# Kernel optimization log

Hardware: AMD Instinct MI355X
Metric: run time of the kernel (lower is better)

The kernel has to match this reference:

```python
import jax, jax.numpy as jnp
import numpy as np

N = 524288   # total spokes
D = 128      # dim_hidden
B = 128      # graphs in batch
H = 64       # hubs per graph (static, num_hubs_type='S')
K = 4        # hubs_per_spoke


def setup_inputs() -> dict:
    key = jax.random.key(0)
    ks = jax.random.split(key, 5)
    x = jax.random.normal(ks[0], (N, D), jnp.float32)
    spoke_init_hub_idx = jax.random.randint(ks[1], (N,), 0, H)
    batch_idx = jnp.sort(jax.random.randint(ks[2], (N,), 0, B))
    s1 = 1.0 / np.sqrt(D)
    s2 = 1.0 / np.sqrt(2 * D)
    W1 = jax.random.uniform(ks[3], (D, 2 * D), jnp.float32, -s1, s1)
    b1 = jnp.zeros((2 * D,), jnp.float32)
    W2 = jax.random.uniform(ks[4], (2 * D, D), jnp.float32, -s2, s2)
    b2 = jnp.zeros((D,), jnp.float32)
    return {"x": x, "spoke_init_hub_idx": spoke_init_hub_idx, "batch_idx": batch_idx,
            "W1": W1, "b1": b1, "W2": W2, "b2": b2}


def reference(x, spoke_init_hub_idx, batch_idx, W1, b1, W2, b2):
    # FeedForward on spokes: Linear -> GELU(exact, torch default) -> Linear
    h = jax.nn.gelu(x @ W1 + b1, approximate=False) @ W2 + b2  # [N, D]

    # batched hub index: local hub idx offset by graph (uniform H hubs/graph)
    gidx = batch_idx * H + spoke_init_hub_idx  # [N]

    # scatter_mean of spoke features into hubs (empty hubs -> 0, as torch scatter_mean)
    sums = jax.ops.segment_sum(h, gidx, num_segments=B * H)                    # [B*H, D]
    cnt = jax.ops.segment_sum(jnp.ones((N,), h.dtype), gidx, num_segments=B * H)
    hub_features = sums / jnp.maximum(cnt, 1.0)[:, None]                       # [B*H, D]

    # assign each spoke to the K hubs closest to its initial hub (within its graph)
    hf = hub_features.reshape(B, H, D)
    d2 = jnp.sum((hf[:, :, None, :] - hf[:, None, :, :]) ** 2, axis=-1)        # [B, H, H]
    _, knn = jax.lax.top_k(-d2, K)                                             # [B, H, K] local hub ids
    hubs_idx = knn[batch_idx, spoke_init_hub_idx] + batch_idx[:, None] * H     # [N, K] global hub ids
    spokes_idx = jnp.repeat(jnp.arange(N), K)
    spokes_hubs_edge_index = jnp.stack([spokes_idx, hubs_idx.reshape(-1)], axis=0)  # [2, N*K]

    return hub_features, spokes_hubs_edge_index
```

## Files before the change

### kernel.cpp

```cpp
#include <hip/hip_runtime.h>
#include <hip/hip_bf16.h>

#define N_SPOKES 524288
#define DIM      128
#define DIM2     256
#define NB       128
#define NH       64
#define BH       8192

#define OUT_HF   0
#define OUT_E0   1048576
#define OUT_E1   3145728

typedef __attribute__((ext_vector_type(8))) short  short8;
typedef __attribute__((ext_vector_type(4))) float  float4v;
typedef __attribute__((ext_vector_type(4))) unsigned short ushort4v;

__device__ inline unsigned short f2bf(float f) {
    __hip_bfloat16 h = __float2bfloat16(f);
    return *reinterpret_cast<unsigned short*>(&h);
}

__device__ inline float gelu_f(float v) {
    float s = v * (1.0f + 0.044715f * v * v);
    float e = __builtin_exp2f(-2.302118131f * s);
    return v * __builtin_amdgcn_rcpf(1.0f + e);
}

__global__ void setup_kernel(const int* __restrict__ batchidx, const int* __restrict__ hubidx,
                             const float* __restrict__ W1,
                             unsigned short* __restrict__ w1t,
                             int* __restrict__ goff, int* __restrict__ cnt) {
    int b = blockIdx.x, tid = threadIdx.x;
    if (b < 2048) {
        int i = b * 256 + tid;
        if (i < N_SPOKES) {
            int bi = batchidx[i];
            int bp = (i == 0) ? -1 : batchidx[i - 1];
            for (int g = bp + 1; g <= bi; ++g) goff[g] = i;
            if (i == N_SPOKES - 1)
                for (int g = bi + 1; g <= NB; ++g) goff[g] = N_SPOKES;
            atomicAdd(&cnt[bi * NH + hubidx[i]], 1);
        }
    } else {
        int idx = (b - 2048) * 256 + tid;
        if (idx < DIM * DIM2) {
            int n = idx >> 7, k = idx & 127;
            w1t[idx] = f2bf(W1[k * DIM2 + n]);
        }
    }
}

__launch_bounds__(512, 2)
__global__ void ffn_fused(const float* __restrict__ x,
                          const int* __restrict__ hubidx,
                          const int* __restrict__ goff,
                          const unsigned short* __restrict__ w1t,
                          const float* __restrict__ b1,
                          float* __restrict__ outbuf,
                          int atomic_mode) {
    __shared__ unsigned short sA[128 * 136];
    __shared__ unsigned short sU[256 * 136];
    __shared__ int sHub[128];

    const int tid  = threadIdx.x;
    const int lane = tid & 63;
    const int w    = tid >> 6;
    const int c_lo = lane & 15;
    const int c_hi = lane >> 4;
    const int wcb  = w * 32;
    const int g      = blockIdx.x >> 1;
    const int cchunk = blockIdx.x & 1;

    const int s = goff[g], e = goff[g + 1];
    const int len = e - s;
    const int cs  = (len + 1) >> 1;
    const int ms  = s + cchunk * cs;
    int me = ms + cs; if (me > e) me = e;
    const int n  = me - ms;
    const int nt = (n + 127) >> 7;

    short8 bfr[2][4];
    #pragma unroll
    for (int n4 = 0; n4 < 2; ++n4)
        #pragma unroll
        for (int k = 0; k < 4; ++k) {
            int col = wcb + n4 * 16 + c_lo;
            bfr[n4][k] = *(const short8*)(w1t + col * DIM + k * 32 + c_hi * 8);
        }
    float bcol[2];
    #pragma unroll
    for (int n4 = 0; n4 < 2; ++n4) bcol[n4] = b1[wcb + n4 * 16 + c_lo];

    float4v hacc[4][2];
    #pragma unroll
    for (int mt = 0; mt < 4; ++mt)
        #pragma unroll
        for (int n4 = 0; n4 < 2; ++n4) hacc[mt][n4] = (float4v){0.f, 0.f, 0.f, 0.f};

    const float4v* x4 = (const float4v*)x;

    float4v pf[8];
    if (nt > 0) {
        #pragma unroll
        for (int it = 0; it < 8; ++it) {
            int f = it * 512 + tid;
            int r = f >> 5;
            int rr = r < n ? r : n - 1;
            pf[it] = x4[(size_t)(ms + rr) * 32 + (f & 31)];
        }
    }

    for (int t = 0; t < nt; ++t) {
        #pragma unroll
        for (int it = 0; it < 8; ++it) {
            int f = it * 512 + tid;
            int row = f >> 5, c4 = f & 31;
            float4v v = pf[it];
            ushort4v u = { f2bf(v.x), f2bf(v.y), f2bf(v.z), f2bf(v.w) };
            *(ushort4v*)&sA[row * 136 + c4 * 4] = u;
        }
        if (tid < 128) {
            int r = t * 128 + tid;
            sHub[tid] = (r < n) ? hubidx[ms + r] : -1;
        }
        __syncthreads();

        if (t + 1 < nt) {
            #pragma unroll
            for (int it = 0; it < 8; ++it) {
                int f = it * 512 + tid;
                int r = (t + 1) * 128 + (f >> 5);
                int rr = r < n ? r : n - 1;
                pf[it] = x4[(size_t)(ms + rr) * 32 + (f & 31)];
            }
        }

        float4v acc[8][2];
        #pragma unroll
        for (int m = 0; m < 8; ++m)
            #pragma unroll
            for (int n4 = 0; n4 < 2; ++n4) acc[m][n4] = (float4v){0.f, 0.f, 0.f, 0.f};

        #pragma unroll
        for (int k = 0; k < 4; ++k)
            #pragma unroll
            for (int m = 0; m < 8; ++m) {
                short8 a = *(const short8*)&sA[(m * 16 + c_lo) * 136 + k * 32 + c_hi * 8];
                #pragma unroll
                for (int n4 = 0; n4 < 2; ++n4)
                    acc[m][n4] = __builtin_amdgcn_mfma_f32_16x16x32_bf16(a, bfr[n4][k], acc[m][n4], 0, 0, 0);
            }

        #pragma unroll
        for (int m = 0; m < 8; ++m) {
            int rbase = m * 16 + c_hi * 4;
            #pragma unroll
            for (int n4 = 0; n4 < 2; ++n4) {
                int col = wcb + n4 * 16 + c_lo;
                float4v a4 = acc[m][n4];
                ushort4v u;
                u.x = f2bf(gelu_f(a4.x + bcol[n4]));
                u.y = f2bf(gelu_f(a4.y + bcol[n4]));
                u.z = f2bf(gelu_f(a4.z + bcol[n4]));
                u.w = f2bf(gelu_f(a4.w + bcol[n4]));
                *(ushort4v*)&sU[col * 136 + rbase] = u;
            }
        }

        #pragma unroll
        for (int ks = 0; ks < 4; ++ks) {
            int4 h0v = *(const int4*)&sHub[ks * 32 + c_hi * 8];
            int4 h1v = *(const int4*)&sHub[ks * 32 + c_hi * 8 + 4];
            short8 aS[4];
            #pragma unroll
            for (int mt = 0; mt < 4; ++mt) {
                int hb = mt * 16 + c_lo;
                short8 a;
                a[0] = (h0v.x == hb) ? (short)0x3F80 : (short)0;
                a[1] = (h0v.y == hb) ? (short)0x3F80 : (short)0;
                a[2] = (h0v.z == hb) ? (short)0x3F80 : (short)0;
                a[3] = (h0v.w == hb) ? (short)0x3F80 : (short)0;
                a[4] = (h1v.x == hb) ? (short)0x3F80 : (short)0;
                a[5] = (h1v.y == hb) ? (short)0x3F80 : (short)0;
                a[6] = (h1v.z == hb) ? (short)0x3F80 : (short)0;
                a[7] = (h1v.w == hb) ? (short)0x3F80 : (short)0;
                aS[mt] = a;
            }
            short8 bU[2];
            #pragma unroll
            for (int n4 = 0; n4 < 2; ++n4) {
                int col = wcb + n4 * 16 + c_lo;
                bU[n4] = *(const short8*)&sU[col * 136 + ks * 32 + c_hi * 8];
            }
            #pragma unroll
            for (int mt = 0; mt < 4; ++mt)
                #pragma unroll
                for (int n4 = 0; n4 < 2; ++n4)
                    hacc[mt][n4] = __builtin_amdgcn_mfma_f32_16x16x32_bf16(aS[mt], bU[n4], hacc[mt][n4], 0, 0, 0);
        }
        __syncthreads();
    }

    #pragma unroll
    for (int mt = 0; mt < 4; ++mt)
        #pragma unroll
        for (int n4 = 0; n4 < 2; ++n4) {
            float4v v = hacc[mt][n4];
            int col = wcb + n4 * 16 + c_lo;
            #pragma unroll
            for (int reg = 0; reg < 4; ++reg) {
                int hub = mt * 16 + c_hi * 4 + reg;
                size_t o = ((size_t)g * NH + hub) * DIM2 + col;
                if (atomic_mode) atomicAdd(&outbuf[o], v[reg]);
                else outbuf[(size_t)cchunk * BH * DIM2 + o] = v[reg];
            }
        }
}

__global__ void hubfeat_kernel(const float* __restrict__ part, int nchunk,
                               const int* __restrict__ cnt,
                               const float* __restrict__ W2, const float* __restrict__ b2,
                               float* __restrict__ out) {
    __shared__ float sSum[16 * 256];
    int tid = threadIdx.x;
    int d   = tid & 127;
    int hh  = tid >> 7;

    for (int i = tid; i < 16 * 256; i += 256) {
        size_t o = (size_t)(blockIdx.x * 16) * DIM2 + i;
        float v = part[o];
        if (nchunk == 2) v += part[(size_t)BH * DIM2 + o];
        sSum[i] = v;
    }
    __syncthreads();

    int h0 = hh * 8;
    float acc[8] = {0.f, 0.f, 0.f, 0.f, 0.f, 0.f, 0.f, 0.f};
    for (int k4 = 0; k4 < 64; ++k4) {
        float w0 = W2[(k4 * 4 + 0) * DIM + d];
        float w1 = W2[(k4 * 4 + 1) * DIM + d];
        float w2 = W2[(k4 * 4 + 2) * DIM + d];
        float w3 = W2[(k4 * 4 + 3) * DIM + d];
        #pragma unroll
        for (int j = 0; j < 8; ++j) {
            float4v sv = *(const float4v*)&sSum[(h0 + j) * 256 + k4 * 4];
            acc[j] += sv.x * w0 + sv.y * w1 + sv.z * w2 + sv.w * w3;
        }
    }
    float b2d = b2[d];
    #pragma unroll
    for (int j = 0; j < 8; ++j) {
        int h = blockIdx.x * 16 + h0 + j;
        float c = (float)cnt[h];
        out[OUT_HF + h * DIM + d] = (acc[j] + c * b2d) / fmaxf(c, 1.0f);
    }
}

__global__ void knn_edges(const float* __restrict__ hf, const int* __restrict__ goff,
                          const int* __restrict__ hubidx, float* __restrict__ out) {
    __shared__ float s[64 * 129];
    __shared__ float d2[64 * 64];
    __shared__ int sK[64 * 4];
    int g = blockIdx.x, tid = threadIdx.x;

    for (int i = tid; i < 64 * 128; i += 256) {
        int r = i >> 7, c = i & 127;
        s[r * 129 + c] = hf[OUT_HF + (g * 64 + r) * DIM + c];
    }
    __syncthreads();

    for (int p = tid; p < 4096; p += 256) {
        int i = p >> 6, j = p & 63;
        float a = 0.f;
        for (int k = 0; k < 128; ++k) {
            float dd = s[i * 129 + k] - s[j * 129 + k];
            a += dd * dd;
        }
        d2[p] = a;
    }
    __syncthreads();

    if (tid < 64) {
        float bv0 = 1e30f, bv1 = 1e30f, bv2 = 1e30f, bv3 = 1e30f;
        int   bi0 = 0,     bi1 = 0,     bi2 = 0,     bi3 = 0;
        for (int j = 0; j < 64; ++j) {
            float v = d2[tid * 64 + j];
            if (v < bv0)      { bv3=bv2; bi3=bi2; bv2=bv1; bi2=bi1; bv1=bv0; bi1=bi0; bv0=v; bi0=j; }
            else if (v < bv1) { bv3=bv2; bi3=bi2; bv2=bv1; bi2=bi1; bv1=v;   bi1=j; }
            else if (v < bv2) { bv3=bv2; bi3=bi2; bv2=v;   bi2=j; }
            else if (v < bv3) { bv3=v;   bi3=j; }
        }
        sK[tid * 4 + 0] = bi0; sK[tid * 4 + 1] = bi1;
        sK[tid * 4 + 2] = bi2; sK[tid * 4 + 3] = bi3;
    }
    __syncthreads();

    int sgs = goff[g], sge = goff[g + 1];
    float gbase = (float)(g * NH);
    for (int i = sgs + tid; i < sge; i += 256) {
        int h = hubidx[i];
        int4 kn = *(const int4*)&sK[h * 4];
        float fi = (float)i;
        float4v o0 = { fi, fi, fi, fi };
        ((float4v*)(out + OUT_E0))[i] = o0;
        float4v o1 = { kn.x + gbase, kn.y + gbase, kn.z + gbase, kn.w + gbase };
        ((float4v*)(out + OUT_E1))[i] = o1;
    }
}

extern "C" void kernel_launch(void* const* d_in, const int* in_sizes, int n_in,
                              void* d_out, int out_size, void* d_ws, size_t ws_size,
                              hipStream_t stream) {
    const float* x        = (const float*)d_in[0];
    const int*   hubidx   = (const int*)d_in[1];
    const int*   batchidx = (const int*)d_in[2];
    const float* W1       = (const float*)d_in[3];
    const float* b1       = (const float*)d_in[4];
    const float* W2       = (const float*)d_in[5];
    const float* b2       = (const float*)d_in[6];
    float* out = (float*)d_out;
    char*  ws  = (char*)d_ws;

    const size_t need_partial = 16879616;
    int atomic_mode = (ws_size < need_partial) ? 1 : 0;

    float*          part;
    int*            cnt;
    unsigned short* w1t;
    int*            goff;
    if (!atomic_mode) {
        part = (float*)ws;
        cnt  = (int*)(ws + 16777216);
        w1t  = (unsigned short*)(ws + 16809984);
        goff = (int*)(ws + 16875520);
    } else {
        part = (float*)ws;
        cnt  = (int*)(ws + 8388608);
        w1t  = (unsigned short*)(ws + 8421376);
        goff = (int*)(ws + 8486912);
    }

    (void)hipMemsetAsync(cnt, 0, 32768, stream);
    if (atomic_mode) (void)hipMemsetAsync(part, 0, 8388608, stream);

    setup_kernel<<<2176, 256, 0, stream>>>(batchidx, hubidx, W1, w1t, goff, cnt);
    ffn_fused   <<<256,  512, 0, stream>>>(x, hubidx, goff, w1t, b1, part, atomic_mode);
    hubfeat_kernel<<<512, 256, 0, stream>>>(part, atomic_mode ? 1 : 2, cnt, W2, b2, out);
    knn_edges   <<<NB,   256, 0, stream>>>(out, goff, hubidx, out);
}
```

Measured before the change: 495.6 us.

## Split each graph into four blocks, shrink LDS, and precompute one-hot scatter matrix

Each graph's spokes are now split across four blocks instead of two, so the grid grows from 256 to 512 blocks and there are four partial-sum buffers for hubfeat to reduce. The first GEMM is restructured into four 32-row sub-slices, so the GELU staging buffer shrinks from 256x136 to 256x40, and launch bounds are raised to allow four blocks per CU. The per-lane one-hot construction for the scatter MFMA is replaced by a shared-memory one-hot matrix that is written and cleared per tile, and hub indices are prefetched into registers. This costs twice the partial-buffer workspace and extra reduction reads, and may add register pressure or spills under the tighter launch bound.

Measured after the change: 554.8 us. 12.0% more time.

```diff
diff --git a/kernel.cpp b/kernel.cpp
--- a/kernel.cpp
+++ b/kernel.cpp
@@ -51,7 +51,7 @@
     }
 }
 
-__launch_bounds__(512, 2)
+__launch_bounds__(512, 4)
 __global__ void ffn_fused(const float* __restrict__ x,
                           const int* __restrict__ hubidx,
                           const int* __restrict__ goff,
@@ -60,8 +60,8 @@
                           float* __restrict__ outbuf,
                           int atomic_mode) {
     __shared__ unsigned short sA[128 * 136];
-    __shared__ unsigned short sU[256 * 136];
-    __shared__ int sHub[128];
+    __shared__ unsigned short sU[256 * 40];
+    __shared__ unsigned short sOne[64 * 136];
 
     const int tid  = threadIdx.x;
     const int lane = tid & 63;
@@ -69,16 +69,16 @@
     const int c_lo = lane & 15;
     const int c_hi = lane >> 4;
     const int wcb  = w * 32;
-    const int g      = blockIdx.x >> 1;
-    const int cchunk = blockIdx.x & 1;
+    const int g      = blockIdx.x >> 2;
+    const int cchunk = blockIdx.x & 3;
 
     const int s = goff[g], e = goff[g + 1];
     const int len = e - s;
-    const int cs  = (len + 1) >> 1;
+    const int cs  = (len + 3) >> 2;
     const int ms  = s + cchunk * cs;
     int me = ms + cs; if (me > e) me = e;
     const int n  = me - ms;
-    const int nt = (n + 127) >> 7;
+    const int nt = (n > 0) ? ((n + 127) >> 7) : 0;
 
     short8 bfr[2][4];
     #pragma unroll
@@ -98,9 +98,13 @@
         #pragma unroll
         for (int n4 = 0; n4 < 2; ++n4) hacc[mt][n4] = (float4v){0.f, 0.f, 0.f, 0.f};
 
+    for (int i = tid; i < 2048; i += 512)
+        *(unsigned long long*)&sOne[(i >> 5) * 136 + (i & 31) * 4] = 0ULL;
+
     const float4v* x4 = (const float4v*)x;
 
     float4v pf[8];
+    int hub_nxt = -1;
     if (nt > 0) {
         #pragma unroll
         for (int it = 0; it < 8; ++it) {
@@ -109,9 +113,12 @@
             int rr = r < n ? r : n - 1;
             pf[it] = x4[(size_t)(ms + rr) * 32 + (f & 31)];
         }
-    }
+        if (tid < 128) hub_nxt = (tid < n) ? hubidx[ms + tid] : -1;
+    }
+    __syncthreads();
 
     for (int t = 0; t < nt; ++t) {
+        const int hub_cur = hub_nxt;
         #pragma unroll
         for (int it = 0; it < 8; ++it) {
             int f = it * 512 + tid;
@@ -120,10 +127,8 @@
             ushort4v u = { f2bf(v.x), f2bf(v.y), f2bf(v.z), f2bf(v.w) };
             *(ushort4v*)&sA[row * 136 + c4 * 4] = u;
         }
-        if (tid < 128) {
-            int r = t * 128 + tid;
-            sHub[tid] = (r < n) ? hubidx[ms + r] : -1;
-        }
+        if (tid < 128 && hub_cur >= 0)
+            sOne[hub_cur * 136 + tid] = (unsigned short)0x3F80;
         __syncthreads();
 
         if (t + 1 < nt) {
@@ -134,65 +139,53 @@
                 int rr = r < n ? r : n - 1;
                 pf[it] = x4[(size_t)(ms + rr) * 32 + (f & 31)];
             }
-        }
-
-        float4v acc[8][2];
-        #pragma unroll
-        for (int m = 0; m < 8; ++m)
-            #pragma unroll
-            for (int n4 = 0; n4 < 2; ++n4) acc[m][n4] = (float4v){0.f, 0.f, 0.f, 0.f};
-
-        #pragma unroll
-        for (int k = 0; k < 4; ++k)
-            #pragma unroll
-            for (int m = 0; m < 8; ++m) {
-                short8 a = *(const short8*)&sA[(m * 16 + c_lo) * 136 + k * 32 + c_hi * 8];
+            if (tid < 128) {
+                int r = (t + 1) * 128 + tid;
+                hub_nxt = (r < n) ? hubidx[ms + r] : -1;
+            }
+        }
+
+        #pragma unroll
+        for (int ks = 0; ks < 4; ++ks) {
+            float4v acc[2][2];
+            #pragma unroll
+            for (int m2 = 0; m2 < 2; ++m2)
                 #pragma unroll
-                for (int n4 = 0; n4 < 2; ++n4)
-                    acc[m][n4] = __builtin_amdgcn_mfma_f32_16x16x32_bf16(a, bfr[n4][k], acc[m][n4], 0, 0, 0);
+                for (int n4 = 0; n4 < 2; ++n4) acc[m2][n4] = (float4v){0.f, 0.f, 0.f, 0.f};
+
+            #pragma unroll
+            for (int k = 0; k < 4; ++k)
+                #pragma unroll
+                for (int m2 = 0; m2 < 2; ++m2) {
+                    short8 a = *(const short8*)&sA[(ks * 32 + m2 * 16 + c_lo) * 136 + k * 32 + c_hi * 8];
+                    acc[m2][0] = __builtin_amdgcn_mfma_f32_16x16x32_bf16(a, bfr[0][k], acc[m2][0], 0, 0, 0);
+                    acc[m2][1] = __builtin_amdgcn_mfma_f32_16x16x32_bf16(a, bfr[1][k], acc[m2][1], 0, 0, 0);
+                }
+
+            #pragma unroll
+            for (int m2 = 0; m2 < 2; ++m2) {
+                int rbase = m2 * 16 + c_hi * 4;
+                #pragma unroll
+                for (int n4 = 0; n4 < 2; ++n4) {
+                    int col = wcb + n4 * 16 + c_lo;
+                    float4v a4 = acc[m2][n4];
+                    ushort4v u;
+                    u.x = f2bf(gelu_f(a4.x + bcol[n4]));
+                    u.y = f2bf(gelu_f(a4.y + bcol[n4]));
+                    u.z = f2bf(gelu_f(a4.z + bcol[n4]));
+                    u.w = f2bf(gelu_f(a4.w + bcol[n4]));
+                    *(ushort4v*)&sU[col * 40 + rbase] = u;
+                }
             }
 
-        #pragma unroll
-        for (int m = 0; m < 8; ++m) {
-            int rbase = m * 16 + c_hi * 4;
-            #pragma unroll
-            for (int n4 = 0; n4 < 2; ++n4) {
-                int col = wcb + n4 * 16 + c_lo;
-                float4v a4 = acc[m][n4];
-                ushort4v u;
-                u.x = f2bf(gelu_f(a4.x + bcol[n4]));
-                u.y = f2bf(gelu_f(a4.y + bcol[n4]));
-                u.z = f2bf(gelu_f(a4.z + bcol[n4]));
-                u.w = f2bf(gelu_f(a4.w + bcol[n4]));
-                *(ushort4v*)&sU[col * 136 + rbase] = u;
-            }
-        }
-
-        #pragma unroll
-        for (int ks = 0; ks < 4; ++ks) {
-            int4 h0v = *(const int4*)&sHub[ks * 32 + c_hi * 8];
-            int4 h1v = *(const int4*)&sHub[ks * 32 + c_hi * 8 + 4];
             short8 aS[4];
             #pragma unroll
-            for (int mt = 0; mt < 4; ++mt) {
-                int hb = mt * 16 + c_lo;
-                short8 a;
-                a[0] = (h0v.x == hb) ? (short)0x3F80 : (short)0;
-                a[1] = (h0v.y == hb) ? (short)0x3F80 : (short)0;
-                a[2] = (h0v.z == hb) ? (short)0x3F80 : (short)0;
-                a[3] = (h0v.w == hb) ? (short)0x3F80 : (short)0;
-                a[4] = (h1v.x == hb) ? (short)0x3F80 : (short)0;
-                a[5] = (h1v.y == hb) ? (short)0x3F80 : (short)0;
-                a[6] = (h1v.z == hb) ? (short)0x3F80 : (short)0;
-                a[7] = (h1v.w == hb) ? (short)0x3F80 : (short)0;
-                aS[mt] = a;
-            }
+            for (int mt = 0; mt < 4; ++mt)
+                aS[mt] = *(const short8*)&sOne[(mt * 16 + c_lo) * 136 + ks * 32 + c_hi * 8];
             short8 bU[2];
             #pragma unroll
-            for (int n4 = 0; n4 < 2; ++n4) {
-                int col = wcb + n4 * 16 + c_lo;
-                bU[n4] = *(const short8*)&sU[col * 136 + ks * 32 + c_hi * 8];
-            }
+            for (int n4 = 0; n4 < 2; ++n4)
+                bU[n4] = *(const short8*)&sU[(wcb + n4 * 16 + c_lo) * 40 + c_hi * 8];
             #pragma unroll
             for (int mt = 0; mt < 4; ++mt)
                 #pragma unroll
@@ -200,6 +193,8 @@
                     hacc[mt][n4] = __builtin_amdgcn_mfma_f32_16x16x32_bf16(aS[mt], bU[n4], hacc[mt][n4], 0, 0, 0);
         }
         __syncthreads();
+        if (tid < 128 && hub_cur >= 0)
+            sOne[hub_cur * 136 + tid] = 0;
     }
 
     #pragma unroll
@@ -229,8 +224,8 @@
 
     for (int i = tid; i < 16 * 256; i += 256) {
         size_t o = (size_t)(blockIdx.x * 16) * DIM2 + i;
-        float v = part[o];
-        if (nchunk == 2) v += part[(size_t)BH * DIM2 + o];
+        float v = 0.f;
+        for (int c = 0; c < nchunk; ++c) v += part[(size_t)c * BH * DIM2 + o];
         sSum[i] = v;
     }
     __syncthreads();
@@ -322,7 +317,7 @@
     float* out = (float*)d_out;
     char*  ws  = (char*)d_ws;
 
-    const size_t need_partial = 16879616;
+    const size_t need_partial = 33654784;
     int atomic_mode = (ws_size < need_partial) ? 1 : 0;
 
     float*          part;
@@ -331,9 +326,9 @@
     int*            goff;
     if (!atomic_mode) {
         part = (float*)ws;
-        cnt  = (int*)(ws + 16777216);
-        w1t  = (unsigned short*)(ws + 16809984);
-        goff = (int*)(ws + 16875520);
+        cnt  = (int*)(ws + 33554432);
+        w1t  = (unsigned short*)(ws + 33587200);
+        goff = (int*)(ws + 33652736);
     } else {
         part = (float*)ws;
         cnt  = (int*)(ws + 8388608);
@@ -345,7 +340,7 @@
     if (atomic_mode) (void)hipMemsetAsync(part, 0, 8388608, stream);
 
     setup_kernel<<<2176, 256, 0, stream>>>(batchidx, hubidx, W1, w1t, goff, cnt);
-    ffn_fused   <<<256,  512, 0, stream>>>(x, hubidx, goff, w1t, b1, part, atomic_mode);
-    hubfeat_kernel<<<512, 256, 0, stream>>>(part, atomic_mode ? 1 : 2, cnt, W2, b2, out);
+    ffn_fused   <<<512,  512, 0, stream>>>(x, hubidx, goff, w1t, b1, part, atomic_mode);
+    hubfeat_kernel<<<512, 256, 0, stream>>>(part, atomic_mode ? 1 : 4, cnt, W2, b2, out);
     knn_edges   <<<NB,   256, 0, stream>>>(out, goff, hubidx, out);
 }
```
